# Kernel optimization log

Measured on AMD Instinct MI355X. Metric: run time of the kernel, lower is better.

Reference implementation:

```python
import jax, jax.numpy as jnp
import numpy as np

B, S, D, DS = 8, 2048, 1024, 128
TEMP = 1.0
C = 8.0


def setup_inputs() -> dict:
    key = jax.random.key(0)
    ks = jax.random.split(key, 8)
    s_in = 1.0 / np.sqrt(D)
    s_st = 1.0 / np.sqrt(DS)
    return {
        "x": jax.random.normal(ks[0], (B, S, D), jnp.float32),
        "W_k": jax.random.normal(ks[1], (DS, D), jnp.float32) * s_in,
        "W_v": jax.random.normal(ks[2], (DS, D), jnp.float32) * s_in,
        "W_q": jax.random.normal(ks[3], (DS, D), jnp.float32) * s_in,
        "W_alpha_w": jax.random.normal(ks[4], (DS, D), jnp.float32) * s_in,
        "W_alpha_b": jnp.zeros((DS,), jnp.float32),
        "lambda_param": jax.random.uniform(ks[5], (DS,), jnp.float32, 4.0, 9.0),
        "W_o": jax.random.normal(ks[6], (D, DS), jnp.float32) * s_st,
        "norm_weight": jnp.ones((DS,), jnp.float32),
    }


def _l2norm(z):
    # matches F.normalize(..., dim=-1) with eps=1e-12
    n = jnp.linalg.norm(z, axis=-1, keepdims=True)
    return z / jnp.maximum(n, 1e-12)


def reference(x, W_k, W_v, W_q, W_alpha_w, W_alpha_b, lambda_param, W_o, norm_weight):
    # projections
    k = _l2norm(x @ W_k.T)                      # [B,S,DS]
    v = x @ W_v.T                               # [B,S,DS]
    q = _l2norm(x @ W_q.T)                      # [B,S,DS]
    r = jax.nn.sigmoid(x @ W_alpha_w.T + W_alpha_b)
    log_a = jnp.log(jax.nn.sigmoid(lambda_param) + 1e-8)  # [DS]
    alpha = jnp.exp(C * r * log_a)              # [B,S,DS], data-dependent decay

    H0 = jnp.zeros((B, DS, DS), x.dtype)        # state indexed [b, k, v]

    def step(H, inp):
        k_t, v_t, q_t, a_t = inp                # each [B,DS]
        # surprise: prediction error against current state
        pred = jnp.einsum('bk,bkv->bv', q_t, H)
        err = jnp.sum((v_t - pred) ** 2, axis=-1, keepdims=True)  # [B,1]
        sur = jax.nn.sigmoid(err / (TEMP + 1e-6))                 # [B,1]
        # delta rule: k (x) v - k (x) (k^T H) = k (x) (v - k^T H)
        k_proj = jnp.einsum('bk,bkv->bv', k_t, H)
        delta = k_t[:, :, None] * (v_t - k_proj)[:, None, :]      # [B,DS,DS]
        a_e = a_t[:, :, None]                                     # decay on k-axis
        H = a_e * H + (1.0 - a_e) * (sur[:, :, None] * delta)
        y = jnp.einsum('bk,bkv->bv', q_t, H)
        return H, y

    seq = (k.transpose(1, 0, 2), v.transpose(1, 0, 2),
           q.transpose(1, 0, 2), alpha.transpose(1, 0, 2))
    _, ys = jax.lax.scan(step, H0, seq)         # ys: [S,B,DS]
    y = ys.transpose(1, 0, 2)                   # [B,S,DS]

    # RMSNorm (computed in fp32, like the torch module)
    yf = y.astype(jnp.float32)
    yn = yf * jax.lax.rsqrt(jnp.mean(yf * yf, axis=-1, keepdims=True) + 1e-6)
    yn = (yn * norm_weight).astype(y.dtype)
    return yn @ W_o.T                           # [B,S,D]
```

## Files before the change

kernel.cpp:

```cpp
#include <hip/hip_runtime.h>
#include <math.h>

#define S_LEN 2048
#define B_SZ 8
#define D_IN 1024
#define DS_ 128
#define INV_TEMP (1.0f/1.000001f)

#define BAR_LDS() asm volatile("s_waitcnt lgkmcnt(0)\n\ts_barrier" ::: "memory")

#define DPPADD(x, ctrl) { int t_ = __builtin_amdgcn_update_dpp( \
    0, __float_as_int(x), ctrl, 0xF, 0xF, false); x += __int_as_float(t_); }
#define ROWSUM(x) { DPPADD(x, 0x128) DPPADD(x, 0x124) DPPADD(x, 0x122) DPPADD(x, 0x121) }
#define ROWSUM4(v4) { ROWSUM(v4.x) ROWSUM(v4.y) ROWSUM(v4.z) ROWSUM(v4.w) }

typedef unsigned int uint2v __attribute__((ext_vector_type(2)));
#define XSUM16(XV) { uint2v r_ = __builtin_amdgcn_permlane16_swap( \
    __float_as_uint(XV), __float_as_uint(XV), false, false); \
    XV = __uint_as_float(r_[0]) + __uint_as_float(r_[1]); }
#define XSUM32(XV) { uint2v r_ = __builtin_amdgcn_permlane32_swap( \
    __float_as_uint(XV), __float_as_uint(XV), false, false); \
    XV = __uint_as_float(r_[0]) + __uint_as_float(r_[1]); }

__global__ __launch_bounds__(256) void proj_gemm(
    const float* __restrict__ X,
    const float* __restrict__ Wk, const float* __restrict__ Wv,
    const float* __restrict__ Wq, const float* __restrict__ Wa,
    float* __restrict__ P)
{
    __shared__ __align__(16) float As[32][132];
    __shared__ __align__(16) float Bs[32][132];
    const int tid = threadIdx.x;
    const int m0 = blockIdx.x * 128;
    const int n0 = blockIdx.y * 128;
    const int sr = tid >> 3;
    const int sk = tid & 7;
    const float* Wbase = (n0 == 0) ? Wk : (n0 == 128) ? Wv : (n0 == 256) ? Wq : Wa;
    const int ty = tid >> 4, tx = tid & 15;

    float acc[8][8];
#pragma unroll
    for (int i = 0; i < 8; i++)
#pragma unroll
        for (int j = 0; j < 8; j++) acc[i][j] = 0.f;

    for (int k0 = 0; k0 < D_IN; k0 += 32) {
#pragma unroll
        for (int i = 0; i < 4; i++) {
            int m = sr + i * 32;
            float4 a4 = *(const float4*)(X + (size_t)(m0 + m) * D_IN + k0 + sk * 4);
            As[sk*4+0][m] = a4.x; As[sk*4+1][m] = a4.y;
            As[sk*4+2][m] = a4.z; As[sk*4+3][m] = a4.w;
            float4 b4 = *(const float4*)(Wbase + (size_t)m * D_IN + k0 + sk * 4);
            Bs[sk*4+0][m] = b4.x; Bs[sk*4+1][m] = b4.y;
            Bs[sk*4+2][m] = b4.z; Bs[sk*4+3][m] = b4.w;
        }
        __syncthreads();
#pragma unroll
        for (int kk = 0; kk < 32; kk++) {
            float4 a0 = *(const float4*)(&As[kk][ty * 8]);
            float4 a1 = *(const float4*)(&As[kk][ty * 8 + 4]);
            float4 b0 = *(const float4*)(&Bs[kk][tx * 8]);
            float4 b1 = *(const float4*)(&Bs[kk][tx * 8 + 4]);
            float a[8] = {a0.x,a0.y,a0.z,a0.w,a1.x,a1.y,a1.z,a1.w};
            float b[8] = {b0.x,b0.y,b0.z,b0.w,b1.x,b1.y,b1.z,b1.w};
#pragma unroll
            for (int i = 0; i < 8; i++)
#pragma unroll
                for (int j = 0; j < 8; j++)
                    acc[i][j] = fmaf(a[i], b[j], acc[i][j]);
        }
        __syncthreads();
    }
#pragma unroll
    for (int i = 0; i < 8; i++) {
        float4 o0; o0.x = acc[i][0]; o0.y = acc[i][1]; o0.z = acc[i][2]; o0.w = acc[i][3];
        float4 o1; o1.x = acc[i][4]; o1.y = acc[i][5]; o1.z = acc[i][6]; o1.w = acc[i][7];
        float* dst = P + (size_t)(m0 + ty * 8 + i) * 512 + n0 + tx * 8;
        *(float4*)(dst) = o0; *(float4*)(dst + 4) = o1;
    }
}

__global__ __launch_bounds__(128) void postproc(
    float* __restrict__ P, float* __restrict__ G,
    const float* __restrict__ bA, const float* __restrict__ lam)
{
    const int tok = blockIdx.x, i = threadIdx.x;
    float* row = P + (size_t)tok * 512;
    float kr = row[i], qr = row[256 + i], rr = row[384 + i];
    float ks = kr * kr, qs = qr * qr;
#pragma unroll
    for (int m = 1; m < 64; m <<= 1) { ks += __shfl_xor(ks, m); qs += __shfl_xor(qs, m); }
    __shared__ float sb[6];
    if ((i & 63) == 0) { sb[(i >> 6) * 2] = ks; sb[(i >> 6) * 2 + 1] = qs; }
    __syncthreads();
    float kinv = 1.0f / fmaxf(sqrtf(sb[0] + sb[2]), 1e-12f);
    float qinv = 1.0f / fmaxf(sqrtf(sb[1] + sb[3]), 1e-12f);
    float kn = kr * kinv, qn = qr * qinv;
    float sr = 1.0f / (1.0f + __expf(-(rr + bA[i])));
    float sl = 1.0f / (1.0f + __expf(-lam[i]));
    float la = logf(sl + 1e-8f);
    float al = __expf(8.0f * sr * la);
    row[i] = kn; row[256 + i] = qn; row[384 + i] = al;
    float gi = qn * (1.0f - al) * kn;
#pragma unroll
    for (int m = 1; m < 64; m <<= 1) gi += __shfl_xor(gi, m);
    if ((i & 63) == 0) sb[4 + (i >> 6)] = gi;
    __syncthreads();
    if (i == 0) G[tok] = sb[4] + sb[5];
}

__global__ __launch_bounds__(512, 2) void recurrence(
    const float* __restrict__ P, const float* __restrict__ G, float* __restrict__ Y)
{
    const int b = blockIdx.x;
    const int tid = threadIdx.x;
    const int c = tid & 15;
    const int vp = tid >> 4;
    const int wave = tid >> 6;
    const int ko = c * 8;
    const int vo = 128 + vp * 4;

    __shared__ __align__(16) float errw[2][8];

    const float* Pb = P + (size_t)b * S_LEN * 512;
    const float* Gb = G + (size_t)b * S_LEN;
    float* Yb = Y + (size_t)b * S_LEN * DS_;

    float4 H0={0,0,0,0},H1={0,0,0,0},H2={0,0,0,0},H3={0,0,0,0},
           H4={0,0,0,0},H5={0,0,0,0},H6={0,0,0,0},H7={0,0,0,0};

    float4 kA0,kA1,qA0,qA1,aA0,aA1,vA; float gA;
    float4 kB0,kB1,qB0,qB1,aB0,aB1,vB; float gB;
    {
        const float* p0 = Pb;
        kA0 = *(const float4*)(p0 + ko);       kA1 = *(const float4*)(p0 + ko + 4);
        qA0 = *(const float4*)(p0 + 256 + ko); qA1 = *(const float4*)(p0 + 256 + ko + 4);
        aA0 = *(const float4*)(p0 + 384 + ko); aA1 = *(const float4*)(p0 + 384 + ko + 4);
        vA  = *(const float4*)(p0 + vo);       gA  = Gb[0];
        const float* p1 = Pb + 512;
        kB0 = *(const float4*)(p1 + ko);       kB1 = *(const float4*)(p1 + ko + 4);
        qB0 = *(const float4*)(p1 + 256 + ko); qB1 = *(const float4*)(p1 + 256 + ko + 4);
        aB0 = *(const float4*)(p1 + 384 + ko); aB1 = *(const float4*)(p1 + 384 + ko + 4);
        vB  = *(const float4*)(p1 + vo);       gB  = Gb[1];
    }

#define DOTJ(qs, ks, zs, Hj) { \
    pr.x = fmaf(qs, Hj.x, pr.x); pr.y = fmaf(qs, Hj.y, pr.y); \
    pr.z = fmaf(qs, Hj.z, pr.z); pr.w = fmaf(qs, Hj.w, pr.w); \
    kp.x = fmaf(ks, Hj.x, kp.x); kp.y = fmaf(ks, Hj.y, kp.y); \
    kp.z = fmaf(ks, Hj.z, kp.z); kp.w = fmaf(ks, Hj.w, kp.w); \
    ya.x = fmaf(zs, Hj.x, ya.x); ya.y = fmaf(zs, Hj.y, ya.y); \
    ya.z = fmaf(zs, Hj.z, ya.z); ya.w = fmaf(zs, Hj.w, ya.w); }

#define UPDJ(as_, ws_, Hj) { \
    Hj.x = fmaf(as_, Hj.x, ws_ * sd.x); Hj.y = fmaf(as_, Hj.y, ws_ * sd.y); \
    Hj.z = fmaf(as_, Hj.z, ws_ * sd.z); Hj.w = fmaf(as_, Hj.w, ws_ * sd.w); }

#define STEP(T, PAR, K0,K1,Q0,Q1,A0,A1,VT,GS) { \
    float4 z0, z1, w0, w1; \
    z0.x = Q0.x * A0.x; z0.y = Q0.y * A0.y; z0.z = Q0.z * A0.z; z0.w = Q0.w * A0.w; \
    z1.x = Q1.x * A1.x; z1.y = Q1.y * A1.y; z1.z = Q1.z * A1.z; z1.w = Q1.w * A1.w; \
    w0.x = fmaf(-K0.x, A0.x, K0.x); w0.y = fmaf(-K0.y, A0.y, K0.y); \
    w0.z = fmaf(-K0.z, A0.z, K0.z); w0.w = fmaf(-K0.w, A0.w, K0.w); \
    w1.x = fmaf(-K1.x, A1.x, K1.x); w1.y = fmaf(-K1.y, A1.y, K1.y); \
    w1.z = fmaf(-K1.z, A1.z, K1.z); w1.w = fmaf(-K1.w, A1.w, K1.w); \
    float4 pr = {0,0,0,0}, kp = {0,0,0,0}, ya = {0,0,0,0}; \
    DOTJ(Q0.x, K0.x, z0.x, H0) DOTJ(Q0.y, K0.y, z0.y, H1) \
    DOTJ(Q0.z, K0.z, z0.z, H2) DOTJ(Q0.w, K0.w, z0.w, H3) \
    DOTJ(Q1.x, K1.x, z1.x, H4) DOTJ(Q1.y, K1.y, z1.y, H5) \
    DOTJ(Q1.z, K1.z, z1.z, H6) DOTJ(Q1.w, K1.w, z1.w, H7) \
    ROWSUM4(pr) ROWSUM4(kp) ROWSUM4(ya) \
    float4 d4; d4.x = VT.x - kp.x; d4.y = VT.y - kp.y; \
    d4.z = VT.z - kp.z; d4.w = VT.w - kp.w; \
    float ex = VT.x - pr.x, ey = VT.y - pr.y, ez = VT.z - pr.z, ew = VT.w - pr.w; \
    float ep = fmaf(ex, ex, fmaf(ey, ey, fmaf(ez, ez, ew * ew))); \
    XSUM16(ep) XSUM32(ep) \
    if ((tid & 63) == 0) errw[PAR][wave] = ep; \
    const float gcur = GS; \
    if ((T) + 2 < S_LEN) { \
        const float* ps_ = Pb + (size_t)((T) + 2) * 512; \
        K0 = *(const float4*)(ps_ + ko);       K1 = *(const float4*)(ps_ + ko + 4); \
        Q0 = *(const float4*)(ps_ + 256 + ko); Q1 = *(const float4*)(ps_ + 256 + ko + 4); \
        VT = *(const float4*)(ps_ + vo); } \
    BAR_LDS(); \
    const float4 ea = *(const float4*)(&errw[PAR][0]); \
    const float4 eb = *(const float4*)(&errw[PAR][4]); \
    float err = ((ea.x + ea.y) + (ea.z + ea.w)) + ((eb.x + eb.y) + (eb.z + eb.w)); \
    float sur = 1.0f / (1.0f + __expf(-err * INV_TEMP)); \
    float4 sd; sd.x = sur * d4.x; sd.y = sur * d4.y; \
    sd.z = sur * d4.z; sd.w = sur * d4.w; \
    if (c == 0) { \
        float sg = sur * gcur; float4 y4; \
        y4.x = fmaf(sg, d4.x, ya.x); y4.y = fmaf(sg, d4.y, ya.y); \
        y4.z = fmaf(sg, d4.z, ya.z); y4.w = fmaf(sg, d4.w, ya.w); \
        *(float4*)(Yb + (size_t)(T) * DS_ + vp * 4) = y4; } \
    if ((T) + 2 < S_LEN) GS = Gb[(T) + 2]; \
    UPDJ(A0.x, w0.x, H0) UPDJ(A0.y, w0.y, H1) \
    UPDJ(A0.z, w0.z, H2) UPDJ(A0.w, w0.w, H3) \
    UPDJ(A1.x, w1.x, H4) UPDJ(A1.y, w1.y, H5) \
    UPDJ(A1.z, w1.z, H6) UPDJ(A1.w, w1.w, H7) \
    if ((T) + 2 < S_LEN) { \
        const float* ps_ = Pb + (size_t)((T) + 2) * 512; \
        A0 = *(const float4*)(ps_ + 384 + ko); A1 = *(const float4*)(ps_ + 384 + ko + 4); } \
}

    for (int t = 0; t < S_LEN; t += 2) {
        STEP(t,     0, kA0,kA1,qA0,qA1,aA0,aA1,vA,gA)
        STEP(t + 1, 1, kB0,kB1,qB0,qB1,aB0,aB1,vB,gB)
    }
#undef DOTJ
#undef UPDJ
#undef STEP
}

__global__ __launch_bounds__(128) void rmsnorm(
    float* __restrict__ Y, const float* __restrict__ nw)
{
    const int tok = blockIdx.x, i = threadIdx.x;
    float y = Y[(size_t)tok * DS_ + i];
    float s = y * y;
#pragma unroll
    for (int m = 1; m < 64; m <<= 1) s += __shfl_xor(s, m);
    __shared__ float sb[2];
    if ((i & 63) == 0) sb[i >> 6] = s;
    __syncthreads();
    float ms = (sb[0] + sb[1]) * (1.0f / 128.0f);
    Y[(size_t)tok * DS_ + i] = y * rsqrtf(ms + 1e-6f) * nw[i];
}

__global__ __launch_bounds__(256) void out_gemm(
    const float* __restrict__ Yn, const float* __restrict__ Wo, float* __restrict__ Out)
{
    __shared__ __align__(16) float As[32][132];
    __shared__ __align__(16) float Bs[32][132];
    const int tid = threadIdx.x;
    const int m0 = blockIdx.x * 128;
    const int n0 = blockIdx.y * 128;
    const int sr = tid >> 3;
    const int sk = tid & 7;
    const int ty = tid >> 4, tx = tid & 15;

    float acc[8][8];
#pragma unroll
    for (int i = 0; i < 8; i++)
#pragma unroll
        for (int j = 0; j < 8; j++) acc[i][j] = 0.f;

    for (int k0 = 0; k0 < DS_; k0 += 32) {
#pragma unroll
        for (int i = 0; i < 4; i++) {
            int m = sr + i * 32;
            float4 a4 = *(const float4*)(Yn + (size_t)(m0 + m) * DS_ + k0 + sk * 4);
            As[sk*4+0][m] = a4.x; As[sk*4+1][m] = a4.y;
            As[sk*4+2][m] = a4.z; As[sk*4+3][m] = a4.w;
            float4 b4 = *(const float4*)(Wo + (size_t)(n0 + m) * DS_ + k0 + sk * 4);
            Bs[sk*4+0][m] = b4.x; Bs[sk*4+1][m] = b4.y;
            Bs[sk*4+2][m] = b4.z; Bs[sk*4+3][m] = b4.w;
        }
        __syncthreads();
#pragma unroll
        for (int kk = 0; kk < 32; kk++) {
            float4 a0 = *(const float4*)(&As[kk][ty * 8]);
            float4 a1 = *(const float4*)(&As[kk][ty * 8 + 4]);
            float4 b0 = *(const float4*)(&Bs[kk][tx * 8]);
            float4 b1 = *(const float4*)(&Bs[kk][tx * 8 + 4]);
            float a[8] = {a0.x,a0.y,a0.z,a0.w,a1.x,a1.y,a1.z,a1.w};
            float b[8] = {b0.x,b0.y,b0.z,b0.w,b1.x,b1.y,b1.z,b1.w};
#pragma unroll
            for (int i = 0; i < 8; i++)
#pragma unroll
                for (int j = 0; j < 8; j++)
                    acc[i][j] = fmaf(a[i], b[j], acc[i][j]);
        }
        __syncthreads();
    }
#pragma unroll
    for (int i = 0; i < 8; i++) {
        float4 o0; o0.x = acc[i][0]; o0.y = acc[i][1]; o0.z = acc[i][2]; o0.w = acc[i][3];
        float4 o1; o1.x = acc[i][4]; o1.y = acc[i][5]; o1.z = acc[i][6]; o1.w = acc[i][7];
        float* dst = Out + (size_t)(m0 + ty * 8 + i) * 1024 + n0 + tx * 8;
        *(float4*)(dst) = o0; *(float4*)(dst + 4) = o1;
    }
}

extern "C" void kernel_launch(void* const* d_in, const int* in_sizes, int n_in,
                              void* d_out, int out_size, void* d_ws, size_t ws_size,
                              hipStream_t stream)
{
    const float* x   = (const float*)d_in[0];
    const float* Wk  = (const float*)d_in[1];
    const float* Wv  = (const float*)d_in[2];
    const float* Wq  = (const float*)d_in[3];
    const float* Waw = (const float*)d_in[4];
    const float* Wab = (const float*)d_in[5];
    const float* lam = (const float*)d_in[6];
    const float* Wo  = (const float*)d_in[7];
    const float* nw  = (const float*)d_in[8];
    float* out = (float*)d_out;

    const size_t NTOK = (size_t)B_SZ * S_LEN;
    float* P  = (float*)d_ws;
    float* G  = P + NTOK * 512;
    float* Y  = G + NTOK;

    proj_gemm<<<dim3(NTOK / 128, 512 / 128), 256, 0, stream>>>(x, Wk, Wv, Wq, Waw, P);
    postproc<<<NTOK, 128, 0, stream>>>(P, G, Wab, lam);
    recurrence<<<B_SZ, 512, 0, stream>>>(P, G, Y);
    rmsnorm<<<NTOK, 128, 0, stream>>>(Y, nw);
    out_gemm<<<dim3(NTOK / 128, 1024 / 128), 256, 0, stream>>>(Y, Wo, out);
}
```

Baseline: 2.744 ms.

## Fuse two recurrence timesteps per barrier via algebraic expansion of second step

Each iteration now handles two timesteps. The second step's predictions, k-projections and outputs are written algebraically in terms of the current state H plus rank-one corrections, and the second surprise error is a quadratic in the first surprise, built from three extra reduced scalars. This halves the number of block barriers and cross-wave LDS reductions per token, at the cost of about twice the FMAs per step, more DPP reductions and higher register pressure. The reordered floating-point arithmetic may drift slightly from the sequential result.

```diff
diff --git a/kernel.cpp b/kernel.cpp
--- a/kernel.cpp
+++ b/kernel.cpp
@@ -121,7 +121,7 @@
     const int ko = c * 8;
     const int vo = 128 + vp * 4;
 
-    __shared__ __align__(16) float errw[2][8];
+    __shared__ __align__(16) float4 errw[2][8];
 
     const float* Pb = P + (size_t)b * S_LEN * 512;
     const float* Gb = G + (size_t)b * S_LEN;
@@ -130,88 +130,127 @@
     float4 H0={0,0,0,0},H1={0,0,0,0},H2={0,0,0,0},H3={0,0,0,0},
            H4={0,0,0,0},H5={0,0,0,0},H6={0,0,0,0},H7={0,0,0,0};
 
-    float4 kA0,kA1,qA0,qA1,aA0,aA1,vA; float gA;
-    float4 kB0,kB1,qB0,qB1,aB0,aB1,vB; float gB;
-    {
-        const float* p0 = Pb;
-        kA0 = *(const float4*)(p0 + ko);       kA1 = *(const float4*)(p0 + ko + 4);
-        qA0 = *(const float4*)(p0 + 256 + ko); qA1 = *(const float4*)(p0 + 256 + ko + 4);
-        aA0 = *(const float4*)(p0 + 384 + ko); aA1 = *(const float4*)(p0 + 384 + ko + 4);
-        vA  = *(const float4*)(p0 + vo);       gA  = Gb[0];
-        const float* p1 = Pb + 512;
-        kB0 = *(const float4*)(p1 + ko);       kB1 = *(const float4*)(p1 + ko + 4);
-        qB0 = *(const float4*)(p1 + 256 + ko); qB1 = *(const float4*)(p1 + 256 + ko + 4);
-        aB0 = *(const float4*)(p1 + 384 + ko); aB1 = *(const float4*)(p1 + 384 + ko + 4);
-        vB  = *(const float4*)(p1 + vo);       gB  = Gb[1];
-    }
-
-#define DOTJ(qs, ks, zs, Hj) { \
-    pr.x = fmaf(qs, Hj.x, pr.x); pr.y = fmaf(qs, Hj.y, pr.y); \
-    pr.z = fmaf(qs, Hj.z, pr.z); pr.w = fmaf(qs, Hj.w, pr.w); \
-    kp.x = fmaf(ks, Hj.x, kp.x); kp.y = fmaf(ks, Hj.y, kp.y); \
-    kp.z = fmaf(ks, Hj.z, kp.z); kp.w = fmaf(ks, Hj.w, kp.w); \
-    ya.x = fmaf(zs, Hj.x, ya.x); ya.y = fmaf(zs, Hj.y, ya.y); \
-    ya.z = fmaf(zs, Hj.z, ya.z); ya.w = fmaf(zs, Hj.w, ya.w); }
-
-#define UPDJ(as_, ws_, Hj) { \
-    Hj.x = fmaf(as_, Hj.x, ws_ * sd.x); Hj.y = fmaf(as_, Hj.y, ws_ * sd.y); \
-    Hj.z = fmaf(as_, Hj.z, ws_ * sd.z); Hj.w = fmaf(as_, Hj.w, ws_ * sd.w); }
-
-#define STEP(T, PAR, K0,K1,Q0,Q1,A0,A1,VT,GS) { \
-    float4 z0, z1, w0, w1; \
-    z0.x = Q0.x * A0.x; z0.y = Q0.y * A0.y; z0.z = Q0.z * A0.z; z0.w = Q0.w * A0.w; \
-    z1.x = Q1.x * A1.x; z1.y = Q1.y * A1.y; z1.z = Q1.z * A1.z; z1.w = Q1.w * A1.w; \
-    w0.x = fmaf(-K0.x, A0.x, K0.x); w0.y = fmaf(-K0.y, A0.y, K0.y); \
-    w0.z = fmaf(-K0.z, A0.z, K0.z); w0.w = fmaf(-K0.w, A0.w, K0.w); \
-    w1.x = fmaf(-K1.x, A1.x, K1.x); w1.y = fmaf(-K1.y, A1.y, K1.y); \
-    w1.z = fmaf(-K1.z, A1.z, K1.z); w1.w = fmaf(-K1.w, A1.w, K1.w); \
-    float4 pr = {0,0,0,0}, kp = {0,0,0,0}, ya = {0,0,0,0}; \
-    DOTJ(Q0.x, K0.x, z0.x, H0) DOTJ(Q0.y, K0.y, z0.y, H1) \
-    DOTJ(Q0.z, K0.z, z0.z, H2) DOTJ(Q0.w, K0.w, z0.w, H3) \
-    DOTJ(Q1.x, K1.x, z1.x, H4) DOTJ(Q1.y, K1.y, z1.y, H5) \
-    DOTJ(Q1.z, K1.z, z1.z, H6) DOTJ(Q1.w, K1.w, z1.w, H7) \
-    ROWSUM4(pr) ROWSUM4(kp) ROWSUM4(ya) \
-    float4 d4; d4.x = VT.x - kp.x; d4.y = VT.y - kp.y; \
-    d4.z = VT.z - kp.z; d4.w = VT.w - kp.w; \
-    float ex = VT.x - pr.x, ey = VT.y - pr.y, ez = VT.z - pr.z, ew = VT.w - pr.w; \
-    float ep = fmaf(ex, ex, fmaf(ey, ey, fmaf(ez, ez, ew * ew))); \
-    XSUM16(ep) XSUM32(ep) \
-    if ((tid & 63) == 0) errw[PAR][wave] = ep; \
-    const float gcur = GS; \
-    if ((T) + 2 < S_LEN) { \
-        const float* ps_ = Pb + (size_t)((T) + 2) * 512; \
-        K0 = *(const float4*)(ps_ + ko);       K1 = *(const float4*)(ps_ + ko + 4); \
-        Q0 = *(const float4*)(ps_ + 256 + ko); Q1 = *(const float4*)(ps_ + 256 + ko + 4); \
-        VT = *(const float4*)(ps_ + vo); } \
+    float4 kA0,kA1,qA0,qA1,aA0,aA1,vA, jA0,jA1,rA0,rA1,bbA0,bbA1,uA;
+    float4 kB0,kB1,qB0,qB1,aB0,aB1,vB, jB0,jB1,rB0,rB1,bbB0,bbB1,uB;
+    float gA,hA,gB,hB;
+
+#define LOADP(S, T) { \
+    const float* p0_ = Pb + (size_t)(T) * 512; \
+    k##S##0 = *(const float4*)(p0_ + ko);       k##S##1 = *(const float4*)(p0_ + ko + 4); \
+    q##S##0 = *(const float4*)(p0_ + 256 + ko); q##S##1 = *(const float4*)(p0_ + 256 + ko + 4); \
+    a##S##0 = *(const float4*)(p0_ + 384 + ko); a##S##1 = *(const float4*)(p0_ + 384 + ko + 4); \
+    v##S    = *(const float4*)(p0_ + vo); \
+    const float* p1_ = p0_ + 512; \
+    j##S##0 = *(const float4*)(p1_ + ko);        j##S##1 = *(const float4*)(p1_ + ko + 4); \
+    r##S##0 = *(const float4*)(p1_ + 256 + ko);  r##S##1 = *(const float4*)(p1_ + 256 + ko + 4); \
+    bb##S##0 = *(const float4*)(p1_ + 384 + ko); bb##S##1 = *(const float4*)(p1_ + 384 + ko + 4); \
+    u##S    = *(const float4*)(p1_ + vo); }
+
+    LOADP(A, 0) LOADP(B, 2)
+    gA = Gb[0]; hA = Gb[1]; gB = Gb[2]; hB = Gb[3];
+
+#define FD(Hj, KX, QX, AX, KY, QY, AY, idx) { \
+    const float wt_ = fmaf(-(KX), (AX), (KX)); \
+    const float qy2_ = (QY) * (AY); \
+    Sqw = fmaf((QY), wt_, Sqw); Skw = fmaf((KY), wt_, Skw); Sqaw = fmaf(qy2_, wt_, Sqaw); \
+    AW[idx] = (AY) * wt_; WY[idx] = fmaf(-(KY), (AY), (KY)); AA[idx] = (AX) * (AY); \
+    const float zt_ = (QX) * (AX); \
+    const float qa_ = (QY) * (AX); \
+    const float ka_ = (KY) * (AX); \
+    const float za_ = qy2_ * (AX); \
+    PR.x = fmaf((QX), Hj.x, PR.x); PR.y = fmaf((QX), Hj.y, PR.y); \
+    PR.z = fmaf((QX), Hj.z, PR.z); PR.w = fmaf((QX), Hj.w, PR.w); \
+    KP.x = fmaf((KX), Hj.x, KP.x); KP.y = fmaf((KX), Hj.y, KP.y); \
+    KP.z = fmaf((KX), Hj.z, KP.z); KP.w = fmaf((KX), Hj.w, KP.w); \
+    YA.x = fmaf(zt_, Hj.x, YA.x); YA.y = fmaf(zt_, Hj.y, YA.y); \
+    YA.z = fmaf(zt_, Hj.z, YA.z); YA.w = fmaf(zt_, Hj.w, YA.w); \
+    PA.x = fmaf(qa_, Hj.x, PA.x); PA.y = fmaf(qa_, Hj.y, PA.y); \
+    PA.z = fmaf(qa_, Hj.z, PA.z); PA.w = fmaf(qa_, Hj.w, PA.w); \
+    KA.x = fmaf(ka_, Hj.x, KA.x); KA.y = fmaf(ka_, Hj.y, KA.y); \
+    KA.z = fmaf(ka_, Hj.z, KA.z); KA.w = fmaf(ka_, Hj.w, KA.w); \
+    YB.x = fmaf(za_, Hj.x, YB.x); YB.y = fmaf(za_, Hj.y, YB.y); \
+    YB.z = fmaf(za_, Hj.z, YB.z); YB.w = fmaf(za_, Hj.w, YB.w); }
+
+#define HUPD(Hj, idx) { \
+    const float u_ = sur * AW[idx]; const float u2_ = sur2 * WY[idx]; \
+    const float aj_ = AA[idx]; \
+    Hj.x = fmaf(aj_, Hj.x, fmaf(u2_, d2.x, u_ * dt.x)); \
+    Hj.y = fmaf(aj_, Hj.y, fmaf(u2_, d2.y, u_ * dt.y)); \
+    Hj.z = fmaf(aj_, Hj.z, fmaf(u2_, d2.z, u_ * dt.z)); \
+    Hj.w = fmaf(aj_, Hj.w, fmaf(u2_, d2.w, u_ * dt.w)); }
+
+#define FSTEP(T, PAR, S) { \
+    float4 PR={0,0,0,0},KP={0,0,0,0},YA={0,0,0,0},PA={0,0,0,0},KA={0,0,0,0},YB={0,0,0,0}; \
+    float Sqw=0.f, Skw=0.f, Sqaw=0.f; \
+    float AW[8], WY[8], AA[8]; \
+    FD(H0, (k##S##0).x, (q##S##0).x, (a##S##0).x, (j##S##0).x, (r##S##0).x, (bb##S##0).x, 0) \
+    FD(H1, (k##S##0).y, (q##S##0).y, (a##S##0).y, (j##S##0).y, (r##S##0).y, (bb##S##0).y, 1) \
+    FD(H2, (k##S##0).z, (q##S##0).z, (a##S##0).z, (j##S##0).z, (r##S##0).z, (bb##S##0).z, 2) \
+    FD(H3, (k##S##0).w, (q##S##0).w, (a##S##0).w, (j##S##0).w, (r##S##0).w, (bb##S##0).w, 3) \
+    FD(H4, (k##S##1).x, (q##S##1).x, (a##S##1).x, (j##S##1).x, (r##S##1).x, (bb##S##1).x, 4) \
+    FD(H5, (k##S##1).y, (q##S##1).y, (a##S##1).y, (j##S##1).y, (r##S##1).y, (bb##S##1).y, 5) \
+    FD(H6, (k##S##1).z, (q##S##1).z, (a##S##1).z, (j##S##1).z, (r##S##1).z, (bb##S##1).z, 6) \
+    FD(H7, (k##S##1).w, (q##S##1).w, (a##S##1).w, (j##S##1).w, (r##S##1).w, (bb##S##1).w, 7) \
+    ROWSUM4(PR) ROWSUM4(KP) ROWSUM4(YA) ROWSUM4(PA) ROWSUM4(KA) ROWSUM4(YB) \
+    ROWSUM(Sqw) ROWSUM(Skw) ROWSUM(Sqaw) \
+    float4 dt; dt.x = (v##S).x - KP.x; dt.y = (v##S).y - KP.y; \
+    dt.z = (v##S).z - KP.z; dt.w = (v##S).w - KP.w; \
+    float ex_ = (v##S).x - PR.x, ey_ = (v##S).y - PR.y, \
+          ez_ = (v##S).z - PR.z, ew_ = (v##S).w - PR.w; \
+    float ep = fmaf(ex_, ex_, fmaf(ey_, ey_, fmaf(ez_, ez_, ew_ * ew_))); \
+    float4 ee; ee.x = (u##S).x - PA.x; ee.y = (u##S).y - PA.y; \
+    ee.z = (u##S).z - PA.z; ee.w = (u##S).w - PA.w; \
+    float4 e2; e2.x = (u##S).x - KA.x; e2.y = (u##S).y - KA.y; \
+    e2.z = (u##S).z - KA.z; e2.w = (u##S).w - KA.w; \
+    float4 Bv; Bv.x = Sqw * dt.x; Bv.y = Sqw * dt.y; \
+    Bv.z = Sqw * dt.z; Bv.w = Sqw * dt.w; \
+    float C0 = fmaf(ee.x, ee.x, fmaf(ee.y, ee.y, fmaf(ee.z, ee.z, ee.w * ee.w))); \
+    float C1 = fmaf(ee.x, Bv.x, fmaf(ee.y, Bv.y, fmaf(ee.z, Bv.z, ee.w * Bv.w))); \
+    float C2 = fmaf(Bv.x, Bv.x, fmaf(Bv.y, Bv.y, fmaf(Bv.z, Bv.z, Bv.w * Bv.w))); \
+    XSUM16(ep) XSUM32(ep) XSUM16(C0) XSUM32(C0) \
+    XSUM16(C1) XSUM32(C1) XSUM16(C2) XSUM32(C2) \
+    if ((tid & 63) == 0) { \
+        float4 pk_; pk_.x = ep; pk_.y = C0; pk_.z = C1; pk_.w = C2; \
+        errw[(PAR)][wave] = pk_; } \
+    if ((T) + 4 < S_LEN) LOADP(S, (T) + 4) \
     BAR_LDS(); \
-    const float4 ea = *(const float4*)(&errw[PAR][0]); \
-    const float4 eb = *(const float4*)(&errw[PAR][4]); \
-    float err = ((ea.x + ea.y) + (ea.z + ea.w)) + ((eb.x + eb.y) + (eb.z + eb.w)); \
-    float sur = 1.0f / (1.0f + __expf(-err * INV_TEMP)); \
-    float4 sd; sd.x = sur * d4.x; sd.y = sur * d4.y; \
-    sd.z = sur * d4.z; sd.w = sur * d4.w; \
+    float4 E0 = errw[(PAR)][0], E1 = errw[(PAR)][1], E2 = errw[(PAR)][2], E3 = errw[(PAR)][3]; \
+    float4 E4 = errw[(PAR)][4], E5 = errw[(PAR)][5], E6 = errw[(PAR)][6], E7 = errw[(PAR)][7]; \
+    float sep = ((E0.x+E1.x)+(E2.x+E3.x))+((E4.x+E5.x)+(E6.x+E7.x)); \
+    float sc0 = ((E0.y+E1.y)+(E2.y+E3.y))+((E4.y+E5.y)+(E6.y+E7.y)); \
+    float sc1 = ((E0.z+E1.z)+(E2.z+E3.z))+((E4.z+E5.z)+(E6.z+E7.z)); \
+    float sc2 = ((E0.w+E1.w)+(E2.w+E3.w))+((E4.w+E5.w)+(E6.w+E7.w)); \
+    float sur = 1.0f / (1.0f + __expf(-sep * INV_TEMP)); \
+    float errN = fmaf(sur, fmaf(sur, sc2, -2.0f * sc1), sc0); \
+    float sur2 = 1.0f / (1.0f + __expf(-errN * INV_TEMP)); \
+    const float gc1_ = g##S; const float gc2_ = h##S; \
+    if ((T) + 4 < S_LEN) { g##S = Gb[(T) + 4]; h##S = Gb[(T) + 5]; } \
+    float ssk_ = sur * Skw; \
+    float4 d2; d2.x = fmaf(-ssk_, dt.x, e2.x); d2.y = fmaf(-ssk_, dt.y, e2.y); \
+    d2.z = fmaf(-ssk_, dt.z, e2.z); d2.w = fmaf(-ssk_, dt.w, e2.w); \
     if (c == 0) { \
-        float sg = sur * gcur; float4 y4; \
-        y4.x = fmaf(sg, d4.x, ya.x); y4.y = fmaf(sg, d4.y, ya.y); \
-        y4.z = fmaf(sg, d4.z, ya.z); y4.w = fmaf(sg, d4.w, ya.w); \
-        *(float4*)(Yb + (size_t)(T) * DS_ + vp * 4) = y4; } \
-    if ((T) + 2 < S_LEN) GS = Gb[(T) + 2]; \
-    UPDJ(A0.x, w0.x, H0) UPDJ(A0.y, w0.y, H1) \
-    UPDJ(A0.z, w0.z, H2) UPDJ(A0.w, w0.w, H3) \
-    UPDJ(A1.x, w1.x, H4) UPDJ(A1.y, w1.y, H5) \
-    UPDJ(A1.z, w1.z, H6) UPDJ(A1.w, w1.w, H7) \
-    if ((T) + 2 < S_LEN) { \
-        const float* ps_ = Pb + (size_t)((T) + 2) * 512; \
-        A0 = *(const float4*)(ps_ + 384 + ko); A1 = *(const float4*)(ps_ + 384 + ko + 4); } \
-}
-
-    for (int t = 0; t < S_LEN; t += 2) {
-        STEP(t,     0, kA0,kA1,qA0,qA1,aA0,aA1,vA,gA)
-        STEP(t + 1, 1, kB0,kB1,qB0,qB1,aB0,aB1,vB,gB)
-    }
-#undef DOTJ
-#undef UPDJ
-#undef STEP
+        float sg_ = sur * gc1_; float4 y1_; \
+        y1_.x = fmaf(sg_, dt.x, YA.x); y1_.y = fmaf(sg_, dt.y, YA.y); \
+        y1_.z = fmaf(sg_, dt.z, YA.z); y1_.w = fmaf(sg_, dt.w, YA.w); \
+        *(float4*)(Yb + (size_t)(T) * DS_ + vp * 4) = y1_; \
+        float sq_ = sur * Sqaw; float sh_ = sur2 * gc2_; float4 y2_; \
+        y2_.x = fmaf(sh_, d2.x, fmaf(sq_, dt.x, YB.x)); \
+        y2_.y = fmaf(sh_, d2.y, fmaf(sq_, dt.y, YB.y)); \
+        y2_.z = fmaf(sh_, d2.z, fmaf(sq_, dt.z, YB.z)); \
+        y2_.w = fmaf(sh_, d2.w, fmaf(sq_, dt.w, YB.w)); \
+        *(float4*)(Yb + (size_t)((T) + 1) * DS_ + vp * 4) = y2_; } \
+    HUPD(H0, 0) HUPD(H1, 1) HUPD(H2, 2) HUPD(H3, 3) \
+    HUPD(H4, 4) HUPD(H5, 5) HUPD(H6, 6) HUPD(H7, 7) \
+}
+
+    for (int t = 0; t < S_LEN; t += 4) {
+        FSTEP(t,     0, A)
+        FSTEP(t + 2, 1, B)
+    }
+#undef FSTEP
+#undef HUPD
+#undef FD
+#undef LOADP
 }
 
 __global__ __launch_bounds__(128) void rmsnorm(
```

Result: slower. 3.360 ms (+22.5%).
